# Kernel optimization log

Hardware: AMD Instinct MI355X
Metric: run time of the kernel (lower is better)

The kernel has to match this reference:

```python
import jax, jax.numpy as jnp
import numpy as np


def setup_inputs() -> dict:
    key = jax.random.key(0)
    ks = jax.random.split(key, 9)
    bs, F, T, d_in, Nh, d_out = 4, 8, 256, 64, 8, 64
    std = 2.0  # gaussian_init_delta_std
    return {
        "X": jax.random.normal(ks[0], (bs, F, T, d_in), dtype=jnp.float32),
        "attention_center": std * jax.random.normal(ks[1], (F, Nh, 1), dtype=jnp.float32),
        "alpha": jax.random.normal(ks[2], (F,), dtype=jnp.float32),
        "W_query": jax.random.normal(ks[3], (F, T, d_in, Nh, 2), dtype=jnp.float32),
        "W_key": jax.random.normal(ks[4], (F, T, d_in, Nh, 2), dtype=jnp.float32),
        "Wkey_": jax.random.normal(ks[5], (F, 2, 2), dtype=jnp.float32),
        "u": jax.random.normal(ks[6], (F, T, 2), dtype=jnp.float32),
        "W": jax.random.normal(ks[7], (F, Nh * d_in, d_out), dtype=jnp.float32),
        "b": jax.random.normal(ks[8], (F, T, d_out), dtype=jnp.float32),
    }


def reference(X, attention_center, alpha, W_query, W_key, Wkey_, u, W, b):
    bs, F, T, d_in = X.shape
    Nh = W_query.shape[3]

    # relative-position features R[t,l] = (l-t)^2, (l-t); identical across F in the original
    rel = (jnp.arange(T)[None, :] - jnp.arange(T)[:, None]).astype(jnp.float32)
    R = jnp.stack([rel ** 2, rel], axis=-1)  # (T,T,2)

    query = jnp.einsum('bftd,ftdhe->bfthe', X, W_query)  # (bs,F,T,Nh,2)
    key = jnp.einsum('bftd,ftdhe->bfthe', X, W_key)      # (bs,F,T,Nh,2)

    r_delta = jnp.einsum('fde,tle->ftld', Wkey_, R)      # (F,T,T,2)

    centers = jnp.concatenate([jnp.ones_like(attention_center), -2.0 * attention_center], axis=-1)  # (F,Nh,2)
    v = -alpha[:, None, None] * centers                  # (F,Nh,2)

    scores = (
        jnp.einsum('bfthe,bflhe->bfthl', query, key)
        + jnp.einsum('bfthe,ftle->bfthl', query, r_delta)
        + jnp.einsum('fle,bfthe->bfthl', u, key)
        + jnp.einsum('fhe,ftle->fthl', v, r_delta)[None]
    )  # (bs,F,T,Nh,T)

    probs = jax.nn.softmax(scores, axis=-1)

    vals = jnp.einsum('bfthl,bfld->bfthd', probs, X)     # (bs,F,T,Nh,d_in)
    vals = vals.reshape(bs, F, T, Nh * d_in)

    return jnp.einsum('bftd,fdo->bfto', vals, W) + b     # (bs,F,T,d_out)
```

## Files before the change

kernel.cpp:

```cpp
#include <hip/hip_runtime.h>
#include <hip/hip_bf16.h>

#define BS 4
#define NF 8
#define NT 256
#define DIN 64
#define NH 8
#define DOUT 64
#define TT 4
#define MROWS 32
#define NCH 64

typedef unsigned short u16;
typedef __attribute__((ext_vector_type(8))) short short8;
typedef __attribute__((ext_vector_type(4))) float f32x4;
typedef __attribute__((ext_vector_type(4))) unsigned int u32x4;

static __device__ __forceinline__ u16 f2bf(float x) {
    __hip_bfloat16 h = __float2bfloat16(x);
    u16 r; __builtin_memcpy(&r, &h, 2); return r;
}
static __device__ __forceinline__ unsigned pk2(float a, float b) {
    return (unsigned)f2bf(a) | ((unsigned)f2bf(b) << 16);
}

__global__ __launch_bounds__(256) void prep_kernel(
    const float* __restrict__ X,
    const float* __restrict__ Wq,
    const float* __restrict__ Wk,
    const float* __restrict__ W,
    float* __restrict__ q,
    float* __restrict__ k,
    u16* __restrict__ XT,
    u16* __restrict__ Wt)
{
    __shared__ float sm[4160];
    const int tid = threadIdx.x;
    const int bid = blockIdx.x;

    if (bid < 2048) {
        const int ft = bid;
        const int f = ft >> 8, t = ft & 255;
        float* sWt = sm;
        float* sX  = sm + 2176;

        float4 a4 = ((const float4*)(Wq + ((size_t)ft << 10)))[tid];
        float4 b4 = ((const float4*)(Wk + ((size_t)ft << 10)))[tid];
        {
            int d = tid >> 2, he = (tid & 3) << 2;
            sWt[(he + 0) * 68 + d] = a4.x;
            sWt[(he + 1) * 68 + d] = a4.y;
            sWt[(he + 2) * 68 + d] = a4.z;
            sWt[(he + 3) * 68 + d] = a4.w;
            sWt[1088 + (he + 0) * 68 + d] = b4.x;
            sWt[1088 + (he + 1) * 68 + d] = b4.y;
            sWt[1088 + (he + 2) * 68 + d] = b4.z;
            sWt[1088 + (he + 3) * 68 + d] = b4.w;
            int xb = tid >> 6, xd = tid & 63;
            sX[tid] = X[(((size_t)((xb * NF + f) * NT + t)) << 6) + xd];
        }
        __syncthreads();

        const int half  = tid & 1;
        const int he    = (tid >> 1) & 15;
        const int b     = (tid >> 5) & 3;
        const int which = tid >> 7;
        const float* wp = sWt + which * 1088 + he * 68 + (half << 5);
        const float* xp = sX + (b << 6) + (half << 5);
        float acc = 0.f;
        #pragma unroll
        for (int j = 0; j < 8; ++j) {
            float4 w = *(const float4*)(wp + (j << 2));
            float4 x = *(const float4*)(xp + (j << 2));
            acc = fmaf(w.x, x.x, acc);
            acc = fmaf(w.y, x.y, acc);
            acc = fmaf(w.z, x.z, acc);
            acc = fmaf(w.w, x.w, acc);
        }
        acc += __shfl_xor(acc, 1);
        if (half == 0) {
            float* outp = which ? k : q;
            outp[(((size_t)((b * NF + f) * NT + t)) << 4) + he] = acc;
        }
    } else if (bid < 2176) {
        const int idx = bid - 2048;
        const int bf = idx >> 2, lc = idx & 3;
        float (*sT)[65] = (float(*)[65])sm;
        #pragma unroll
        for (int i = 0; i < 16; ++i) {
            int l = i * 4 + (tid >> 6), d = tid & 63;
            sT[l][d] = X[(((size_t)(bf * NT) + lc * 64 + l) << 6) + d];
        }
        __syncthreads();
        #pragma unroll
        for (int i = 0; i < 16; ++i) {
            int d = i * 4 + (tid >> 6), l = tid & 63;
            XT[(((size_t)(bf * 64) + d) << 8) + lc * 64 + l] = f2bf(sT[l][d]);
        }
    } else {
        const int idx = bid - 2176;
        const int f = idx >> 3, kc = idx & 7;
        float (*sT)[65] = (float(*)[65])sm;
        #pragma unroll
        for (int i = 0; i < 16; ++i) {
            int kk = i * 4 + (tid >> 6), o = tid & 63;
            sT[kk][o] = W[(((size_t)(f * 512) + kc * 64 + kk) << 6) + o];
        }
        __syncthreads();
        #pragma unroll
        for (int i = 0; i < 16; ++i) {
            int o = i * 4 + (tid >> 6), kk = tid & 63;
            Wt[(((size_t)(f * 64) + o) << 9) + kc * 64 + kk] = f2bf(sT[kk][o]);
        }
    }
}

__global__ __launch_bounds__(256, 4) void attn_kernel(
    const float* __restrict__ ac,
    const float* __restrict__ alpha,
    const float* __restrict__ Wkey_,
    const float* __restrict__ u,
    const float* __restrict__ bias,
    const float* __restrict__ q,
    const float* __restrict__ kws,
    const u16* __restrict__ XT,
    const u16* __restrict__ Wt,
    float* __restrict__ out)
{
    __shared__ u16  sP[MROWS * 256];
    __shared__ float sKU[4608];
    __shared__ float sRed[MROWS * 16];
    __shared__ float sM[MROWS];
    __shared__ float sInvS[MROWS];

    const int tid = threadIdx.x;
    const int bid = blockIdx.x;
    const int ch = bid & 63;
    const int f  = (bid >> 6) & 7;
    const int b  = bid >> 9;
    const int bf = b * NF + f;
    const int t0 = ch * TT;

    {
        const float4* k4 = (const float4*)(kws + ((size_t)bf << 12));
        float4* d4 = (float4*)sKU;
        #pragma unroll
        for (int i = 0; i < 4; ++i) d4[i * 256 + tid] = k4[i * 256 + tid];
        if (tid < 128) ((float4*)(sKU + 4096))[tid] = ((const float4*)(u + f * 512))[tid];
    }
    __syncthreads();

    const int h  = tid & 7;
    const int tp = (tid >> 3) & 1;
    const int lg = tid >> 4;
    const int t_a = t0 + tp * 2, t_b = t_a + 1;
    const int m_a = tp * 16 + h, m_b = m_a + 8;
    const int lbase = lg * 16;

    float q0a, q1a, kt0a, kt1a, c2a, c1a;
    float q0b, q1b, kt0b, kt1b, c2b, c1b;
    {
        float al = alpha[f];
        float acv = ac[f * 8 + h];
        float wk0 = Wkey_[f * 4],     wk1 = Wkey_[f * 4 + 1];
        float wk2 = Wkey_[f * 4 + 2], wk3 = Wkey_[f * 4 + 3];
        float2 qa = *(const float2*)(q + ((size_t)(bf * NT + t_a) << 4) + (h << 1));
        float2 qb = *(const float2*)(q + ((size_t)(bf * NT + t_b) << 4) + (h << 1));
        q0a = qa.x; q1a = qa.y; q0b = qb.x; q1b = qb.y;
        kt0a = sKU[t_a * 16 + h * 2]; kt1a = sKU[t_a * 16 + h * 2 + 1];
        kt0b = sKU[t_b * 16 + h * 2]; kt1b = sKU[t_b * 16 + h * 2 + 1];
        float a0 = q0a - al, a1 = q1a + 2.f * al * acv;
        c2a = a0 * wk0 + a1 * wk2; c1a = a0 * wk1 + a1 * wk3;
        a0 = q0b - al; a1 = q1b + 2.f * al * acv;
        c2b = a0 * wk0 + a1 * wk2; c1b = a0 * wk1 + a1 * wk3;
    }

    float sA[16], sB[16];
    float mxa = -1e30f, mxb = -1e30f;
    {
        float rela = (float)(lbase - t_a);
        #pragma unroll
        for (int j = 0; j < 16; ++j) {
            int l = lbase + j;
            float2 K = *(const float2*)(sKU + l * 16 + h * 2);
            float2 U = *(const float2*)(sKU + 4096 + l * 2);
            float relb = rela - 1.f;
            float sa = (c2a * rela + c1a) * rela;
            sa = fmaf(q0a, K.x, sa); sa = fmaf(q1a, K.y, sa);
            sa = fmaf(kt0a, U.x, sa); sa = fmaf(kt1a, U.y, sa);
            float sb = (c2b * relb + c1b) * relb;
            sb = fmaf(q0b, K.x, sb); sb = fmaf(q1b, K.y, sb);
            sb = fmaf(kt0b, U.x, sb); sb = fmaf(kt1b, U.y, sb);
            sA[j] = sa; sB[j] = sb;
            mxa = fmaxf(mxa, sa); mxb = fmaxf(mxb, sb);
            rela += 1.f;
        }
    }
    sRed[m_a * 16 + lg] = mxa;
    sRed[m_b * 16 + lg] = mxb;
    __syncthreads();
    if (tid < MROWS) {
        const float4* r4 = (const float4*)(sRed + tid * 16);
        float4 r0 = r4[0], r1 = r4[1], r2 = r4[2], r3 = r4[3];
        float mm = fmaxf(fmaxf(fmaxf(r0.x, r0.y), fmaxf(r0.z, r0.w)),
                         fmaxf(fmaxf(r1.x, r1.y), fmaxf(r1.z, r1.w)));
        mm = fmaxf(mm, fmaxf(fmaxf(fmaxf(r2.x, r2.y), fmaxf(r2.z, r2.w)),
                             fmaxf(fmaxf(r3.x, r3.y), fmaxf(r3.z, r3.w))));
        sM[tid] = mm;
    }
    __syncthreads();

    {
        const float Ma = sM[m_a], Mb = sM[m_b];
        float suma = 0.f, sumb = 0.f;
        unsigned pka[4], pkb[4];
        float epa = 0.f, epb = 0.f;
        #pragma unroll
        for (int j = 0; j < 16; ++j) {
            float ea = __expf(sA[j] - Ma), eb = __expf(sB[j] - Mb);
            suma += ea; sumb += eb;
            if ((j & 1) == 0) { epa = ea; epb = eb; }
            else { pka[(j & 7) >> 1] = pk2(epa, ea); pkb[(j & 7) >> 1] = pk2(epb, eb); }
            if ((j & 7) == 7) {
                int chunk = lg * 2 + (j >> 3);
                int pa = chunk ^ h;
                int pb = chunk ^ (h + 8);
                *(u32x4*)&sP[m_a * 256 + pa * 8] = (u32x4){pka[0], pka[1], pka[2], pka[3]};
                *(u32x4*)&sP[m_b * 256 + pb * 8] = (u32x4){pkb[0], pkb[1], pkb[2], pkb[3]};
            }
        }
        sRed[m_a * 16 + lg] = suma;
        sRed[m_b * 16 + lg] = sumb;
    }

    const int wv   = tid >> 6;
    const int lane = tid & 63;
    const int quad = lane >> 4;
    const int ln   = lane & 15;
    const int mh   = wv & 1;
    const int nh   = wv >> 1;
    const u16* xb = XT + ((size_t)bf << 14);
    short8 nb0, nb1;
    {
        int l2 = quad * 8;
        nb0 = *(const short8*)(xb + (nh * 32 + ln) * 256 + l2);
        nb1 = *(const short8*)(xb + (nh * 32 + 16 + ln) * 256 + l2);
    }
    __syncthreads();
    if (tid < MROWS) {
        const float4* r4 = (const float4*)(sRed + tid * 16);
        float4 r0 = r4[0], r1 = r4[1], r2 = r4[2], r3 = r4[3];
        float ss = ((r0.x + r0.y) + (r0.z + r0.w)) + ((r1.x + r1.y) + (r1.z + r1.w))
                 + ((r2.x + r2.y) + (r2.z + r2.w)) + ((r3.x + r3.y) + (r3.z + r3.w));
        sInvS[tid] = 1.f / ss;
    }
    __syncthreads();

    f32x4 acc0 = {0.f, 0.f, 0.f, 0.f}, acc1 = acc0;
    #pragma unroll
    for (int ks = 0; ks < 8; ++ks) {
        short8 b0 = nb0, b1 = nb1;
        if (ks < 7) {
            int l2 = (ks + 1) * 32 + quad * 8;
            nb0 = *(const short8*)(xb + (nh * 32 + ln) * 256 + l2);
            nb1 = *(const short8*)(xb + (nh * 32 + 16 + ln) * 256 + l2);
        }
        int phys = (ks * 4 + quad) ^ ln;
        short8 a = *(const short8*)&sP[(mh * 16 + ln) * 256 + phys * 8];
        acc0 = __builtin_amdgcn_mfma_f32_16x16x32_bf16(a, b0, acc0, 0, 0, 0);
        acc1 = __builtin_amdgcn_mfma_f32_16x16x32_bf16(a, b1, acc1, 0, 0, 0);
    }

    u16* sVals = (u16*)sKU;
    #pragma unroll
    for (int reg = 0; reg < 4; ++reg) {
        int mg = mh * 16 + quad * 4 + reg;
        float inv = sInvS[mg];
        int tl = mg >> 3, hh = mg & 7;
        u16* dst = sVals + tl * 520 + hh * 64 + nh * 32 + ln;
        dst[0]  = f2bf(acc0[reg] * inv);
        dst[16] = f2bf(acc1[reg] * inv);
    }
    const u16* wb = Wt + ((size_t)(f * 64 + wv * 16 + ln) << 9);
    short8 nw = *(const short8*)(wb + quad * 8);
    __syncthreads();

    f32x4 oacc = {0.f, 0.f, 0.f, 0.f};
    #pragma unroll
    for (int ks = 0; ks < 16; ++ks) {
        short8 bw = nw;
        if (ks < 15) nw = *(const short8*)(wb + (ks + 1) * 32 + quad * 8);
        short8 a = *(const short8*)(sVals + ln * 520 + ks * 32 + quad * 8);
        oacc = __builtin_amdgcn_mfma_f32_16x16x32_bf16(a, bw, oacc, 0, 0, 0);
    }
    {
        int o = wv * 16 + ln;
        #pragma unroll
        for (int reg = 0; reg < 4; ++reg) {
            int tl = quad * 4 + reg;
            if (tl < TT) {
                int tg = t0 + tl;
                out[((size_t)(bf * NT + tg) << 6) + o] =
                    oacc[reg] + bias[((size_t)(f * NT + tg) << 6) + o];
            }
        }
    }
}

extern "C" void kernel_launch(void* const* d_in, const int* in_sizes, int n_in,
                              void* d_out, int out_size, void* d_ws, size_t ws_size,
                              hipStream_t stream) {
    const float* X     = (const float*)d_in[0];
    const float* ac    = (const float*)d_in[1];
    const float* alpha = (const float*)d_in[2];
    const float* Wq    = (const float*)d_in[3];
    const float* Wk    = (const float*)d_in[4];
    const float* Wkey_ = (const float*)d_in[5];
    const float* u     = (const float*)d_in[6];
    const float* W     = (const float*)d_in[7];
    const float* bb    = (const float*)d_in[8];
    float* out = (float*)d_out;

    float* qws = (float*)d_ws;
    float* kws = qws + 131072;
    u16* XT = (u16*)(kws + 131072);
    u16* Wt = XT + 524288;

    hipLaunchKernelGGL(prep_kernel, dim3(2240), dim3(256), 0, stream,
                       X, Wq, Wk, W, qws, kws, XT, Wt);
    hipLaunchKernelGGL(attn_kernel, dim3(BS * NF * NCH), dim3(256), 0, stream,
                       ac, alpha, Wkey_, u, bb, qws, kws, XT, Wt, out);
}
```

Baseline: 118.4 us.

## Store keys transposed and read K/u directly from global, shrinking shared memory

The prep kernel now writes key projections transposed per (bf, head-component) so the attention kernel can load contiguous float4 vectors of K and u straight from global/L2 instead of first staging the whole 16KB K tile and u into shared memory behind a barrier. The P and vals buffers are merged into one aliased shared array, with an extra barrier before vals are written over P. This cuts LDS use per block, which may raise occupancy, and removes the upfront staging load and its sync. In exchange each thread issues redundant global loads that depend on cache hits, and the transposed key write in prep is strided.

```diff
diff --git a/kernel.cpp b/kernel.cpp
--- a/kernel.cpp
+++ b/kernel.cpp
@@ -30,7 +30,7 @@
     const float* __restrict__ Wk,
     const float* __restrict__ W,
     float* __restrict__ q,
-    float* __restrict__ k,
+    float* __restrict__ kT,
     u16* __restrict__ XT,
     u16* __restrict__ Wt)
 {
@@ -79,8 +79,9 @@
         }
         acc += __shfl_xor(acc, 1);
         if (half == 0) {
-            float* outp = which ? k : q;
-            outp[(((size_t)((b * NF + f) * NT + t)) << 4) + he] = acc;
+            int bf = b * NF + f;
+            if (which) kT[(((size_t)(bf * 16 + he)) << 8) + t] = acc;
+            else       q[(((size_t)(bf * NT + t)) << 4) + he] = acc;
         }
     } else if (bid < 2176) {
         const int idx = bid - 2048;
@@ -122,13 +123,12 @@
     const float* __restrict__ u,
     const float* __restrict__ bias,
     const float* __restrict__ q,
-    const float* __restrict__ kws,
+    const float* __restrict__ kT,
     const u16* __restrict__ XT,
     const u16* __restrict__ Wt,
     float* __restrict__ out)
 {
-    __shared__ u16  sP[MROWS * 256];
-    __shared__ float sKU[4608];
+    __shared__ __align__(16) u16 sPV[8320];
     __shared__ float sRed[MROWS * 16];
     __shared__ float sM[MROWS];
     __shared__ float sInvS[MROWS];
@@ -141,21 +141,16 @@
     const int bf = b * NF + f;
     const int t0 = ch * TT;
 
-    {
-        const float4* k4 = (const float4*)(kws + ((size_t)bf << 12));
-        float4* d4 = (float4*)sKU;
-        #pragma unroll
-        for (int i = 0; i < 4; ++i) d4[i * 256 + tid] = k4[i * 256 + tid];
-        if (tid < 128) ((float4*)(sKU + 4096))[tid] = ((const float4*)(u + f * 512))[tid];
-    }
-    __syncthreads();
-
     const int h  = tid & 7;
     const int tp = (tid >> 3) & 1;
     const int lg = tid >> 4;
     const int t_a = t0 + tp * 2, t_b = t_a + 1;
     const int m_a = tp * 16 + h, m_b = m_a + 8;
     const int lbase = lg * 16;
+
+    const float* kT0 = kT + ((size_t)bf << 12) + ((h * 2) << 8);
+    const float* kT1 = kT0 + 256;
+    const float* up  = u + (f << 9);
 
     float q0a, q1a, kt0a, kt1a, c2a, c1a;
     float q0b, q1b, kt0b, kt1b, c2b, c1b;
@@ -167,8 +162,8 @@
         float2 qa = *(const float2*)(q + ((size_t)(bf * NT + t_a) << 4) + (h << 1));
         float2 qb = *(const float2*)(q + ((size_t)(bf * NT + t_b) << 4) + (h << 1));
         q0a = qa.x; q1a = qa.y; q0b = qb.x; q1b = qb.y;
-        kt0a = sKU[t_a * 16 + h * 2]; kt1a = sKU[t_a * 16 + h * 2 + 1];
-        kt0b = sKU[t_b * 16 + h * 2]; kt1b = sKU[t_b * 16 + h * 2 + 1];
+        kt0a = kT0[t_a]; kt1a = kT1[t_a];
+        kt0b = kT0[t_b]; kt1b = kT1[t_b];
         float a0 = q0a - al, a1 = q1a + 2.f * al * acv;
         c2a = a0 * wk0 + a1 * wk2; c1a = a0 * wk1 + a1 * wk3;
         a0 = q0b - al; a1 = q1b + 2.f * al * acv;
@@ -177,23 +172,29 @@
 
     float sA[16], sB[16];
     float mxa = -1e30f, mxb = -1e30f;
-    {
-        float rela = (float)(lbase - t_a);
-        #pragma unroll
-        for (int j = 0; j < 16; ++j) {
-            int l = lbase + j;
-            float2 K = *(const float2*)(sKU + l * 16 + h * 2);
-            float2 U = *(const float2*)(sKU + 4096 + l * 2);
+    #pragma unroll
+    for (int g = 0; g < 4; ++g) {
+        const int l0 = lbase + g * 4;
+        float4 K0 = *(const float4*)(kT0 + l0);
+        float4 K1 = *(const float4*)(kT1 + l0);
+        float4 U0 = *(const float4*)(up + (l0 << 1));
+        float4 U1 = *(const float4*)(up + (l0 << 1) + 4);
+        float k0s[4] = {K0.x, K0.y, K0.z, K0.w};
+        float k1s[4] = {K1.x, K1.y, K1.z, K1.w};
+        float u0s[4] = {U0.x, U0.z, U1.x, U1.z};
+        float u1s[4] = {U0.y, U0.w, U1.y, U1.w};
+        #pragma unroll
+        for (int j = 0; j < 4; ++j) {
+            float rela = (float)(l0 + j - t_a);
             float relb = rela - 1.f;
             float sa = (c2a * rela + c1a) * rela;
-            sa = fmaf(q0a, K.x, sa); sa = fmaf(q1a, K.y, sa);
-            sa = fmaf(kt0a, U.x, sa); sa = fmaf(kt1a, U.y, sa);
+            sa = fmaf(q0a, k0s[j], sa); sa = fmaf(q1a, k1s[j], sa);
+            sa = fmaf(kt0a, u0s[j], sa); sa = fmaf(kt1a, u1s[j], sa);
             float sb = (c2b * relb + c1b) * relb;
-            sb = fmaf(q0b, K.x, sb); sb = fmaf(q1b, K.y, sb);
-            sb = fmaf(kt0b, U.x, sb); sb = fmaf(kt1b, U.y, sb);
-            sA[j] = sa; sB[j] = sb;
+            sb = fmaf(q0b, k0s[j], sb); sb = fmaf(q1b, k1s[j], sb);
+            sb = fmaf(kt0b, u0s[j], sb); sb = fmaf(kt1b, u1s[j], sb);
+            sA[g * 4 + j] = sa; sB[g * 4 + j] = sb;
             mxa = fmaxf(mxa, sa); mxb = fmaxf(mxb, sb);
-            rela += 1.f;
         }
     }
     sRed[m_a * 16 + lg] = mxa;
@@ -210,6 +211,7 @@
     }
     __syncthreads();
 
+    u16* sP = sPV;
     {
         const float Ma = sM[m_a], Mb = sM[m_b];
         float suma = 0.f, sumb = 0.f;
@@ -270,19 +272,26 @@
         acc0 = __builtin_amdgcn_mfma_f32_16x16x32_bf16(a, b0, acc0, 0, 0, 0);
         acc1 = __builtin_amdgcn_mfma_f32_16x16x32_bf16(a, b1, acc1, 0, 0, 0);
     }
-
-    u16* sVals = (u16*)sKU;
-    #pragma unroll
-    for (int reg = 0; reg < 4; ++reg) {
-        int mg = mh * 16 + quad * 4 + reg;
-        float inv = sInvS[mg];
-        int tl = mg >> 3, hh = mg & 7;
-        u16* dst = sVals + tl * 520 + hh * 64 + nh * 32 + ln;
-        dst[0]  = f2bf(acc0[reg] * inv);
-        dst[16] = f2bf(acc1[reg] * inv);
-    }
+    float inv0 = sInvS[mh * 16 + quad * 4 + 0];
+    float inv1 = sInvS[mh * 16 + quad * 4 + 1];
+    float inv2 = sInvS[mh * 16 + quad * 4 + 2];
+    float inv3 = sInvS[mh * 16 + quad * 4 + 3];
     const u16* wb = Wt + ((size_t)(f * 64 + wv * 16 + ln) << 9);
     short8 nw = *(const short8*)(wb + quad * 8);
+    __syncthreads();
+
+    u16* sVals = sPV;
+    {
+        float invs[4] = {inv0, inv1, inv2, inv3};
+        #pragma unroll
+        for (int reg = 0; reg < 4; ++reg) {
+            int mg = mh * 16 + quad * 4 + reg;
+            int tl = mg >> 3, hh = mg & 7;
+            u16* dst = sVals + tl * 520 + hh * 64 + nh * 32 + ln;
+            dst[0]  = f2bf(acc0[reg] * invs[reg]);
+            dst[16] = f2bf(acc1[reg] * invs[reg]);
+        }
+    }
     __syncthreads();
 
     f32x4 oacc = {0.f, 0.f, 0.f, 0.f};
@@ -322,12 +331,12 @@
     float* out = (float*)d_out;
 
     float* qws = (float*)d_ws;
-    float* kws = qws + 131072;
-    u16* XT = (u16*)(kws + 131072);
+    float* kTp = qws + 131072;
+    u16* XT = (u16*)(kTp + 131072);
     u16* Wt = XT + 524288;
 
     hipLaunchKernelGGL(prep_kernel, dim3(2240), dim3(256), 0, stream,
-                       X, Wq, Wk, W, qws, kws, XT, Wt);
+                       X, Wq, Wk, W, qws, kTp, XT, Wt);
     hipLaunchKernelGGL(attn_kernel, dim3(BS * NF * NCH), dim3(256), 0, stream,
-                       ac, alpha, Wkey_, u, bb, qws, kws, XT, Wt, out);
-}
+                       ac, alpha, Wkey_, u, bb, qws, kTp, XT, Wt, out);
+}
```

Measured after the change: 125.5 us. +6.0%, slower.
